# Optimization experiments

Hardware: AMD Instinct MI355X
Metric: run time of the kernel (lower is better)

## Reference

```python
import jax, jax.numpy as jnp
import numpy as np

# Constants from the torch module
S_DECAY = 0.95    # sentence_decay
P_DECAY = 0.99    # paragraph_decay
D_DECAY = 0.999   # document_decay
ALPHA = 0.1       # delta_update alpha for sentence/paragraph
DOC_ALPHA = 0.05  # delta_update alpha for document
BETA = 1.0
PARA_GROUP = 5    # sentences per paragraph
EPS = 1e-12       # F.normalize eps


def _normalize(x):
    # matches torch.nn.functional.normalize(x, dim=-1)
    return x / jnp.maximum(jnp.linalg.norm(x, axis=-1, keepdims=True), EPS)


def _delta_step(M, kn, v, alpha, beta):
    # M: [H, dk, dv]; kn: [dk] (already L2-normalized); v: [dv]
    # M_new = M @ (I - alpha * kn kn^T) + beta * kn v^T   (erase matrix is symmetric,
    # so the einsum 'hkv,hkj->hjv' form equals this rank-1 update -- no dk x dk matrix needed)
    kTM = jnp.einsum('k,hkv->hv', kn, M)                       # [H, dv]
    return M - alpha * kn[None, :, None] * kTM[:, None, :] \
             + beta * (kn[:, None] * v[None, :])[None, :, :]


def _scan_updates(M0, K, V, decay, alpha, beta):
    # Streaming delta-rule: per step, decay then erase/write.
    def step(M, kv):
        k, v = kv
        M = M * decay
        M = _delta_step(M, _normalize(k), v, alpha, beta)
        return M, None
    M, _ = jax.lax.scan(step, M0, (K, V))
    return M


def setup_inputs() -> dict:
    key = jax.random.key(0)
    ks = jax.random.split(key, 7)
    T, d_emb, d_k, d_v, H = 1000, 768, 256, 256, 8
    emb = jax.random.normal(ks[0], (T, d_emb), dtype=jnp.float32)
    q = jax.random.normal(ks[1], (d_k,), dtype=jnp.float32)
    W_k = jax.random.normal(ks[2], (d_emb, d_k), dtype=jnp.float32) * 0.02
    b_k = jax.random.normal(ks[3], (d_k,), dtype=jnp.float32) * 0.02
    W_v = jax.random.normal(ks[4], (d_emb, d_v), dtype=jnp.float32) * 0.02
    b_v = jax.random.normal(ks[5], (d_v,), dtype=jnp.float32) * 0.02
    M_sent0 = jnp.zeros((H, d_k, d_v), dtype=jnp.float32)
    M_para0 = jnp.zeros((H, d_k, d_v), dtype=jnp.float32)
    M_doc0 = jnp.zeros((H, d_k, d_v), dtype=jnp.float32)
    return {"emb": emb, "q": q, "W_k": W_k, "b_k": b_k, "W_v": W_v, "b_v": b_v,
            "M_sent0": M_sent0, "M_para0": M_para0, "M_doc0": M_doc0}


def reference(emb, q, W_k, b_k, W_v, b_v, M_sent0, M_para0, M_doc0):
    T, d_emb = emb.shape
    # Level 1: sentence memory -- one delta update per sentence embedding
    K = emb @ W_k + b_k            # [T, dk]
    V = emb @ W_v + b_v            # [T, dv]
    M_sent = _scan_updates(M_sent0, K, V, S_DECAY, ALPHA, BETA)
    # Level 2: paragraph memory -- mean of each group of 5 sentence embeddings
    para_emb = emb.reshape(T // PARA_GROUP, PARA_GROUP, d_emb).mean(axis=1)
    PK = para_emb @ W_k + b_k
    PV = para_emb @ W_v + b_v
    M_para = _scan_updates(M_para0, PK, PV, P_DECAY, ALPHA, BETA)
    # Level 3: document memory -- single update from paragraph-memory statistics
    doc_k = M_para.mean(axis=0).mean(axis=-1)   # [dk]
    doc_v = M_para.mean(axis=0).mean(axis=0)    # [dv]
    M_doc = M_doc0 * D_DECAY
    M_doc = _delta_step(M_doc, _normalize(doc_k), doc_v, DOC_ALPHA, BETA)
    # recall(q, level='all')
    qn = _normalize(q)
    def recall(M):
        return jnp.einsum('hkv,k->hv', M, qn).mean(axis=0)   # [dv]
    return 0.2 * recall(M_sent) + 0.3 * recall(M_para) + 0.5 * recall(M_doc)
```

## Files before the change

kernel.cpp:

```cpp
#include <hip/hip_runtime.h>
#include <hip/hip_bf16.h>

#define ALPHA   0.1f
#define S_DECAY 0.95f
#define P_DECAY 0.99f
#define D_EMB   768
#define DK      256

template<int ctrl, int row_mask>
__device__ __forceinline__ float dpp_add(float x) {
    int y = __builtin_amdgcn_update_dpp(0, __float_as_int(x), ctrl, row_mask, 0xF, true);
    return x + __int_as_float(y);
}

template<int N>
__device__ __forceinline__ void wave_allred_arr(float (&x)[N]) {
#pragma unroll
    for (int n = 0; n < N; ++n) x[n] = dpp_add<0xB1,  0xF>(x[n]);
#pragma unroll
    for (int n = 0; n < N; ++n) x[n] = dpp_add<0x4E,  0xF>(x[n]);
#pragma unroll
    for (int n = 0; n < N; ++n) x[n] = dpp_add<0x141, 0xF>(x[n]);
#pragma unroll
    for (int n = 0; n < N; ++n) x[n] = dpp_add<0x140, 0xF>(x[n]);
#pragma unroll
    for (int n = 0; n < N; ++n) x[n] = dpp_add<0x142, 0xA>(x[n]);
#pragma unroll
    for (int n = 0; n < N; ++n) x[n] = dpp_add<0x143, 0xC>(x[n]);
#pragma unroll
    for (int n = 0; n < N; ++n)
        x[n] = __int_as_float(__builtin_amdgcn_readlane(__float_as_int(x[n]), 63));
}

__device__ __forceinline__ float dot4v(const float4& a, const float4& b) {
    float t0 = a.x * b.x; t0 = fmaf(a.y, b.y, t0);
    float t1 = a.z * b.z; t1 = fmaf(a.w, b.w, t1);
    return t0 + t1;
}

__device__ __forceinline__ float rl(float x, int lane) {
    return __int_as_float(__builtin_amdgcn_readlane(__float_as_int(x), lane));
}

__global__ __launch_bounds__(256) void prep_kernel(
    const float* __restrict__ emb,
    const float* __restrict__ Wk, const float* __restrict__ bk,
    const float* __restrict__ Wv, const float* __restrict__ bv,
    float* __restrict__ K, float* __restrict__ V, float* __restrict__ USrev,
    float* __restrict__ out, int T)
{
    const int tid = threadIdx.x;
    const int bid = blockIdx.x;
    const int NBLK = (T / 4) * 2;
    if (bid >= NBLK) {
        const int PADS = ((T + 63) / 64) * 64;
        for (int i = tid; i < (PADS - T) * DK; i += 256) USrev[(size_t)T * DK + i] = 0.f;
        out[tid] = 0.f;
        return;
    }
    const int mat = bid & 1;
    const int r0  = (bid >> 1) * 4;

    __shared__ float se[4][D_EMB];
    __shared__ float s_red[4][4];

    const float4* emb4 = reinterpret_cast<const float4*>(emb);
#pragma unroll
    for (int r = 0; r < 4; ++r) {
        if (tid < D_EMB / 4)
            reinterpret_cast<float4*>(se[r])[tid] = emb4[(size_t)(r0 + r) * (D_EMB / 4) + tid];
    }
    __syncthreads();

    const float* Wp = mat ? Wv : Wk;
    const float* bp = mat ? bv : bk;
    const int j = tid;

    float a0 = 0.f, a1 = 0.f, a2 = 0.f, a3 = 0.f;
    float c0 = Wp[j],        c1 = Wp[j + DK],     c2 = Wp[j + 2*DK], c3 = Wp[j + 3*DK];
    float p0 = Wp[j + 4*DK], p1 = Wp[j + 5*DK],   p2 = Wp[j + 6*DK], p3 = Wp[j + 7*DK];

    for (int d = 0; d < D_EMB; d += 4) {
        int dn = d + 8; if (dn >= D_EMB) dn = 0;
        const float* wn = Wp + (size_t)dn * DK + j;
        float n0 = wn[0], n1 = wn[DK], n2 = wn[2*DK], n3 = wn[3*DK];

        float4 e0 = *reinterpret_cast<const float4*>(&se[0][d]);
        float4 e1 = *reinterpret_cast<const float4*>(&se[1][d]);
        float4 e2 = *reinterpret_cast<const float4*>(&se[2][d]);
        float4 e3 = *reinterpret_cast<const float4*>(&se[3][d]);

        a0 = fmaf(e0.x, c0, a0); a0 = fmaf(e0.y, c1, a0);
        a0 = fmaf(e0.z, c2, a0); a0 = fmaf(e0.w, c3, a0);
        a1 = fmaf(e1.x, c0, a1); a1 = fmaf(e1.y, c1, a1);
        a1 = fmaf(e1.z, c2, a1); a1 = fmaf(e1.w, c3, a1);
        a2 = fmaf(e2.x, c0, a2); a2 = fmaf(e2.y, c1, a2);
        a2 = fmaf(e2.z, c2, a2); a2 = fmaf(e2.w, c3, a2);
        a3 = fmaf(e3.x, c0, a3); a3 = fmaf(e3.y, c1, a3);
        a3 = fmaf(e3.z, c2, a3); a3 = fmaf(e3.w, c3, a3);

        c0 = p0; c1 = p1; c2 = p2; c3 = p3;
        p0 = n0; p1 = n1; p2 = n2; p3 = n3;
    }

    float bj = bp[j];
    float o0 = a0 + bj, o1 = a1 + bj, o2 = a2 + bj, o3 = a3 + bj;
    float* dst = mat ? V : K;
    dst[(size_t)(r0 + 0) * DK + j] = o0;
    dst[(size_t)(r0 + 1) * DK + j] = o1;
    dst[(size_t)(r0 + 2) * DK + j] = o2;
    dst[(size_t)(r0 + 3) * DK + j] = o3;

    if (mat == 0) {
        const int wave = tid >> 6, l = tid & 63;
        float red[4] = { o0*o0, o1*o1, o2*o2, o3*o3 };
        wave_allred_arr(red);
        if (l == 0) {
            s_red[wave][0] = red[0]; s_red[wave][1] = red[1];
            s_red[wave][2] = red[2]; s_red[wave][3] = red[3];
        }
        __syncthreads();
        float t0 = s_red[0][0] + s_red[1][0] + s_red[2][0] + s_red[3][0];
        float t1 = s_red[0][1] + s_red[1][1] + s_red[2][1] + s_red[3][1];
        float t2 = s_red[0][2] + s_red[1][2] + s_red[2][2] + s_red[3][2];
        float t3 = s_red[0][3] + s_red[1][3] + s_red[2][3] + s_red[3][3];
        USrev[(size_t)(T - 1 - (r0 + 0)) * DK + j] = o0 * (1.0f / fmaxf(sqrtf(t0), 1e-12f));
        USrev[(size_t)(T - 1 - (r0 + 1)) * DK + j] = o1 * (1.0f / fmaxf(sqrtf(t1), 1e-12f));
        USrev[(size_t)(T - 1 - (r0 + 2)) * DK + j] = o2 * (1.0f / fmaxf(sqrtf(t2), 1e-12f));
        USrev[(size_t)(T - 1 - (r0 + 3)) * DK + j] = o3 * (1.0f / fmaxf(sqrtf(t3), 1e-12f));
    }
}

__global__ __launch_bounds__(256) void ufill_kernel(
    const float* __restrict__ K, const float* __restrict__ V,
    float* __restrict__ UPrev, float* __restrict__ UPfwd,
    float* __restrict__ PV, float* __restrict__ SVv, float* __restrict__ F1,
    int P, int NCP)
{
    __shared__ float s_pd[64];
    __shared__ float4 s_f1w[4][64];
    const int tid = threadIdx.x, wv = tid >> 6, l = tid & 63;
    const int bid = blockIdx.x;
    const int type = (bid < NCP) ? 1 : 2;
    const int m = (type == 1) ? bid : bid - NCP;

    if (tid < 64) s_pd[tid] = powf(P_DECAY, (float)tid);
    __syncthreads();

    const float4* K4 = reinterpret_cast<const float4*>(K);

    if (type == 1) {
        for (int ii = 0; ii < 16; ++ii) {
            int i = wv * 16 + ii;
            int p = P - 1 - (64 * m + i);
            float4 u = make_float4(0.f, 0.f, 0.f, 0.f);
            if (p >= 0) {
                float4 pk = make_float4(0.f, 0.f, 0.f, 0.f);
#pragma unroll
                for (int s = 0; s < 5; ++s) {
                    float4 k4 = K4[(size_t)(5 * p + s) * 64 + l];
                    pk.x += k4.x; pk.y += k4.y; pk.z += k4.z; pk.w += k4.w;
                }
                pk.x *= 0.2f; pk.y *= 0.2f; pk.z *= 0.2f; pk.w *= 0.2f;
                float red[1] = { dot4v(pk, pk) };
                wave_allred_arr(red);
                float inv = 1.0f / fmaxf(sqrtf(red[0]), 1e-12f);
                u = make_float4(pk.x * inv, pk.y * inv, pk.z * inv, pk.w * inv);
            }
            reinterpret_cast<float4*>(UPrev)[(size_t)(64 * m + i) * 64 + l] = u;
        }
    } else {
        const float4* V4 = reinterpret_cast<const float4*>(V);
        float4 f1p = make_float4(0.f, 0.f, 0.f, 0.f);
        for (int ii = 0; ii < 16; ++ii) {
            int i = wv * 16 + ii;
            int p = 64 * m + i;
            float4 u = make_float4(0.f, 0.f, 0.f, 0.f);
            float sv = 0.f;
            if (p < P) {
                float4 pk = make_float4(0.f, 0.f, 0.f, 0.f);
                float4 pv = make_float4(0.f, 0.f, 0.f, 0.f);
#pragma unroll
                for (int s = 0; s < 5; ++s) {
                    float4 k4 = K4[(size_t)(5 * p + s) * 64 + l];
                    float4 v4 = V4[(size_t)(5 * p + s) * 64 + l];
                    pk.x += k4.x; pk.y += k4.y; pk.z += k4.z; pk.w += k4.w;
                    pv.x += v4.x; pv.y += v4.y; pv.z += v4.z; pv.w += v4.w;
                }
                pk.x *= 0.2f; pk.y *= 0.2f; pk.z *= 0.2f; pk.w *= 0.2f;
                pv.x *= 0.2f; pv.y *= 0.2f; pv.z *= 0.2f; pv.w *= 0.2f;
                reinterpret_cast<float4*>(PV)[(size_t)p * 64 + l] = pv;
                float red[2] = { dot4v(pk, pk), pv.x + pv.y + pv.z + pv.w };
                wave_allred_arr(red);
                float inv = 1.0f / fmaxf(sqrtf(red[0]), 1e-12f);
                u = make_float4(pk.x * inv, pk.y * inv, pk.z * inv, pk.w * inv);
                sv = red[1];
            }
            reinterpret_cast<float4*>(UPfwd)[(size_t)(64 * m + i) * 64 + l] = u;
            if (l == 0) SVv[64 * m + i] = sv;
            float f = s_pd[63 - i] * sv;
            f1p.x = fmaf(f, u.x, f1p.x); f1p.y = fmaf(f, u.y, f1p.y);
            f1p.z = fmaf(f, u.z, f1p.z); f1p.w = fmaf(f, u.w, f1p.w);
        }
        s_f1w[wv][l] = f1p;
        __syncthreads();
        if (wv == 0) {
            float4 a = s_f1w[0][l], b = s_f1w[1][l], c = s_f1w[2][l], d = s_f1w[3][l];
            float4 tot = make_float4(a.x+b.x+c.x+d.x, a.y+b.y+c.y+d.y,
                                     a.z+b.z+c.z+d.z, a.w+b.w+c.w+d.w);
            reinterpret_cast<float4*>(F1)[(size_t)m * 64 + l] = tot;
        }
    }
}

#define GS_STRIDE 260
__global__ __launch_bounds__(256) void gram_kernel(
    const float* __restrict__ USrev, const float* __restrict__ UPrev,
    const float* __restrict__ UPfwd, float* __restrict__ Agram,
    int NCS, int NCP)
{
    __shared__ float sAr[16 * GS_STRIDE];
    __shared__ float s_pd[64];
    const int tid = threadIdx.x;
    const int chunk = blockIdx.x >> 2;
    const int slab  = blockIdx.x & 3;
    int type, m;
    if (chunk < NCS)            { type = 0; m = chunk; }
    else if (chunk < NCS + NCP) { type = 1; m = chunk - NCS; }
    else                        { type = 2; m = chunk - NCS - NCP; }
    const float* Ug = (type == 0) ? USrev + (size_t)m * 64 * DK
                    : (type == 1) ? UPrev + (size_t)m * 64 * DK
                                  : UPfwd + (size_t)m * 64 * DK;
    const float4* Ug4 = reinterpret_cast<const float4*>(Ug);

    for (int idx = tid; idx < 16 * 64; idx += 256) {
        int r = idx >> 6, c4 = idx & 63;
        float4 t = Ug4[(size_t)(slab * 16 + r) * 64 + c4];
        *reinterpret_cast<float4*>(&sAr[r * GS_STRIDE + 4 * c4]) = t;
    }
    if (tid < 64) s_pd[tid] = powf(P_DECAY, (float)tid);
    __syncthreads();

    const int ti = tid & 15;
    const int tj = tid >> 4;
    const int gi = slab * 16 + ti;
    const int j0 = tj * 4;

    const float4* B0 = Ug4 + (size_t)(j0 + 0) * 64;
    const float4* B1 = Ug4 + (size_t)(j0 + 1) * 64;
    const float4* B2 = Ug4 + (size_t)(j0 + 2) * 64;
    const float4* B3 = Ug4 + (size_t)(j0 + 3) * 64;

    float g0 = 0.f, g1 = 0.f, g2 = 0.f, g3 = 0.f;
    for (int k4 = 0; k4 < 64; ++k4) {
        float4 a  = *reinterpret_cast<const float4*>(&sAr[ti * GS_STRIDE + 4 * k4]);
        float4 b0 = B0[k4], b1 = B1[k4], b2 = B2[k4], b3 = B3[k4];
        g0 += dot4v(a, b0); g1 += dot4v(a, b1);
        g2 += dot4v(a, b2); g3 += dot4v(a, b3);
    }

    float4 outv;
    outv.x = (j0 + 0 < gi) ? (ALPHA * g0 * ((type == 2) ? s_pd[gi - (j0 + 0)] : 1.f)) : 0.f;
    outv.y = (j0 + 1 < gi) ? (ALPHA * g1 * ((type == 2) ? s_pd[gi - (j0 + 1)] : 1.f)) : 0.f;
    outv.z = (j0 + 2 < gi) ? (ALPHA * g2 * ((type == 2) ? s_pd[gi - (j0 + 2)] : 1.f)) : 0.f;
    outv.w = (j0 + 3 < gi) ? (ALPHA * g3 * ((type == 2) ? s_pd[gi - (j0 + 3)] : 1.f)) : 0.f;
    reinterpret_cast<float4*>(Agram + (size_t)chunk * 4096)[gi * 16 + tj] = outv;
}

__global__ __launch_bounds__(256) void inv_kernel(
    float* __restrict__ AinvT, const float* __restrict__ SVv,
    float* __restrict__ biasF, int NCS, int NCP)
{
    __shared__ float sA[64 * 65];
    __shared__ float sX[64 * 65];
    __shared__ float s_sv[64];
    const int tid = threadIdx.x, wv = tid >> 6, l = tid & 63;
    const int bid = blockIdx.x;
    int type, m;
    if (bid < NCS)            { type = 0; m = bid; }
    else if (bid < NCS + NCP) { type = 1; m = bid - NCS; }
    else                      { type = 2; m = bid - NCS - NCP; }

    float* Ag = AinvT + (size_t)bid * 4096;
    for (int idx = tid; idx < 4096; idx += 256)
        sA[(idx >> 6) * 65 + (idx & 63)] = Ag[idx];
    if (type == 2 && tid < 64) s_sv[tid] = SVv[m * 64 + tid];
    __syncthreads();

    if (type == 2 && wv == 0) {
        float dotb = 0.f;
#pragma unroll
        for (int jj = 0; jj < 64; ++jj)
            dotb = fmaf(sA[l * 65 + jj], s_sv[jj], dotb);
        biasF[m * 64 + l] = dotb * (1.0f / ALPHA);
    }

    {
        const int base = wv * 16;
        float x[16];
#pragma unroll
        for (int r = 0; r < 16; ++r) x[r] = (base + r == l) ? 1.f : 0.f;
        for (int s = 0; s < 4; ++s) {
            if (wv == s) {
#pragma unroll
                for (int i = 1; i < 16; ++i)
#pragma unroll
                    for (int jj = 0; jj < 16; ++jj)
                        if (jj < i)
                            x[i] = fmaf(-sA[(base + i) * 65 + (base + jj)], x[jj], x[i]);
#pragma unroll
                for (int r = 0; r < 16; ++r) sX[(base + r) * 65 + l] = x[r];
            }
            __syncthreads();
            if (wv > s) {
#pragma unroll
                for (int i = 0; i < 16; ++i) {
                    float xi = sX[(s * 16 + i) * 65 + l];
#pragma unroll
                    for (int r = 0; r < 16; ++r)
                        x[r] = fmaf(-sA[(base + r) * 65 + (s * 16 + i)], xi, x[r]);
                }
            }
        }
    }
    __syncthreads();

    for (int idx = tid; idx < 4096; idx += 256) {
        int jcol = idx >> 6, irow = idx & 63;
        Ag[idx] = sX[irow * 65 + jcol];
    }
}

__global__ __launch_bounds__(512) void solve_kernel(
    const float* __restrict__ USrev, const float* __restrict__ UPrev,
    const float* __restrict__ UPfwd, const float* __restrict__ AinvT,
    const float* __restrict__ F1, const float* __restrict__ biasF,
    const float* __restrict__ q,
    float* __restrict__ BS, float* __restrict__ BPB1, float* __restrict__ BPB2,
    float* __restrict__ gscal, int NCS, int NCP)
{
    __shared__ float s_cp[8][64], s_cp2[8][64];
    __shared__ float4 s_part[8][64], s_part2[8][64];
    __shared__ float s_powd[65];
    const int tid = threadIdx.x, wave = tid >> 6, l = tid & 63;
    const int wb = wave * 8;
    if (tid <= 64) s_powd[tid] = powf(P_DECAY, (float)tid);

    float4 q4 = reinterpret_cast<const float4*>(q)[l];
    float qs[1] = { dot4v(q4, q4) };
    wave_allred_arr(qs);
    float qinv = 1.0f / fmaxf(sqrtf(qs[0]), 1e-12f);
    float4 qn = make_float4(q4.x * qinv, q4.y * qinv, q4.z * qinv, q4.w * qinv);
    __syncthreads();

    if (blockIdx.x == 0) {
        float4 w1 = qn;
        const float4* U4 = reinterpret_cast<const float4*>(USrev);
        float4 curU[8]; float curX[8];
#pragma unroll
        for (int r = 0; r < 8; ++r) {
            curU[r] = U4[(size_t)(wb + r) * 64 + l];
            curX[r] = AinvT[(size_t)(wb + r) * 64 + l];
        }
        for (int m = 0; m < NCS; ++m) {
            float4 nxtU[8]; float nxtX[8];
            if (m + 1 < NCS) {
#pragma unroll
                for (int r = 0; r < 8; ++r) {
                    nxtU[r] = U4[(size_t)(m + 1) * 4096 + (size_t)(wb + r) * 64 + l];
                    nxtX[r] = AinvT[(size_t)(m + 1) * 4096 + (size_t)(wb + r) * 64 + l];
                }
            }
            float d[8];
#pragma unroll
            for (int r = 0; r < 8; ++r) d[r] = dot4v(curU[r], w1);
            wave_allred_arr(d);
            if (l == 0) {
#pragma unroll
                for (int r = 0; r < 8; ++r) BS[m * 64 + wb + r] = d[r];
            }
            float cp = 0.f;
#pragma unroll
            for (int r = 0; r < 8; ++r) cp = fmaf(curX[r], d[r], cp);
            s_cp[wave][l] = cp;
            __syncthreads();
            float cl = 0.f;
#pragma unroll
            for (int w = 0; w < 8; ++w) cl += s_cp[w][l];
            float4 part = make_float4(0.f, 0.f, 0.f, 0.f);
#pragma unroll
            for (int r = 0; r < 8; ++r) {
                float ci = rl(cl, wb + r);
                part.x = fmaf(ci, curU[r].x, part.x); part.y = fmaf(ci, curU[r].y, part.y);
                part.z = fmaf(ci, curU[r].z, part.z); part.w = fmaf(ci, curU[r].w, part.w);
            }
            s_part[wave][l] = part;
            __syncthreads();
            float4 s = make_float4(0.f, 0.f, 0.f, 0.f);
#pragma unroll
            for (int w = 0; w < 8; ++w) {
                float4 p = s_part[w][l];
                s.x += p.x; s.y += p.y; s.z += p.z; s.w += p.w;
            }
            w1.x = fmaf(-ALPHA, s.x, w1.x); w1.y = fmaf(-ALPHA, s.y, w1.y);
            w1.z = fmaf(-ALPHA, s.z, w1.z); w1.w = fmaf(-ALPHA, s.w, w1.w);
            if (m + 1 < NCS) {
#pragma unroll
                for (int r = 0; r < 8; ++r) { curU[r] = nxtU[r]; curX[r] = nxtX[r]; }
            }
        }
    } else {
        {
            float4 w1 = qn;
            float4 w2 = make_float4(1.f, 1.f, 1.f, 1.f);
            const float4* U4 = reinterpret_cast<const float4*>(UPrev);
            float4 curU[8]; float curX[8];
#pragma unroll
            for (int r = 0; r < 8; ++r) {
                curU[r] = U4[(size_t)(wb + r) * 64 + l];
                curX[r] = AinvT[(size_t)NCS * 4096 + (size_t)(wb + r) * 64 + l];
            }
            for (int m = 0; m < NCP; ++m) {
                float4 nxtU[8]; float nxtX[8];
                if (m + 1 < NCP) {
#pragma unroll
                    for (int r = 0; r < 8; ++r) {
                        nxtU[r] = U4[(size_t)(m + 1) * 4096 + (size_t)(wb + r) * 64 + l];
                        nxtX[r] = AinvT[(size_t)(NCS + m + 1) * 4096 + (size_t)(wb + r) * 64 + l];
                    }
                }
                float d[16];
#pragma unroll
                for (int r = 0; r < 8; ++r) {
                    d[r]     = dot4v(curU[r], w1);
                    d[8 + r] = dot4v(curU[r], w2);
                }
                wave_allred_arr(d);
                if (l == 0) {
#pragma unroll
                    for (int r = 0; r < 8; ++r) {
                        BPB1[m * 64 + wb + r] = d[r];
                        BPB2[m * 64 + wb + r] = d[8 + r];
                    }
                }
                float cp1 = 0.f, cp2 = 0.f;
#pragma unroll
                for (int r = 0; r < 8; ++r) {
                    cp1 = fmaf(curX[r], d[r], cp1);
                    cp2 = fmaf(curX[r], d[8 + r], cp2);
                }
                s_cp[wave][l] = cp1; s_cp2[wave][l] = cp2;
                __syncthreads();
                float cl1 = 0.f, cl2 = 0.f;
#pragma unroll
                for (int w = 0; w < 8; ++w) { cl1 += s_cp[w][l]; cl2 += s_cp2[w][l]; }
                float4 p1 = make_float4(0.f,0.f,0.f,0.f), p2 = make_float4(0.f,0.f,0.f,0.f);
#pragma unroll
                for (int r = 0; r < 8; ++r) {
                    float c1 = rl(cl1, wb + r), c2 = rl(cl2, wb + r);
                    p1.x = fmaf(c1, curU[r].x, p1.x); p1.y = fmaf(c1, curU[r].y, p1.y);
                    p1.z = fmaf(c1, curU[r].z, p1.z); p1.w = fmaf(c1, curU[r].w, p1.w);
                    p2.x = fmaf(c2, curU[r].x, p2.x); p2.y = fmaf(c2, curU[r].y, p2.y);
                    p2.z = fmaf(c2, curU[r].z, p2.z); p2.w = fmaf(c2, curU[r].w, p2.w);
                }
                s_part[wave][l] = p1; s_part2[wave][l] = p2;
                __syncthreads();
                float4 s1 = make_float4(0.f,0.f,0.f,0.f), s2 = make_float4(0.f,0.f,0.f,0.f);
#pragma unroll
                for (int w = 0; w < 8; ++w) {
                    float4 a = s_part[w][l];  float4 b = s_part2[w][l];
                    s1.x += a.x; s1.y += a.y; s1.z += a.z; s1.w += a.w;
                    s2.x += b.x; s2.y += b.y; s2.z += b.z; s2.w += b.w;
                }
                w1.x = fmaf(-ALPHA, s1.x, w1.x); w1.y = fmaf(-ALPHA, s1.y, w1.y);
                w1.z = fmaf(-ALPHA, s1.z, w1.z); w1.w = fmaf(-ALPHA, s1.w, w1.w);
                w2.x = fmaf(-ALPHA, s2.x, w2.x); w2.y = fmaf(-ALPHA, s2.y, w2.y);
                w2.z = fmaf(-ALPHA, s2.z, w2.z); w2.w = fmaf(-ALPHA, s2.w, w2.w);
                if (m + 1 < NCP) {
#pragma unroll
                    for (int r = 0; r < 8; ++r) { curU[r] = nxtU[r]; curX[r] = nxtX[r]; }
                }
            }
        }
        __syncthreads();
        float4 y = make_float4(0.f, 0.f, 0.f, 0.f);
        {
            const float4* U4 = reinterpret_cast<const float4*>(UPfwd);
            float4 curU[8]; float curX[8];
#pragma unroll
            for (int r = 0; r < 8; ++r) {
                curU[r] = U4[(size_t)(wb + r) * 64 + l];
                curX[r] = AinvT[(size_t)(NCS + NCP) * 4096 + (size_t)(wb + r) * 64 + l];
            }
            for (int m = 0; m < NCP; ++m) {
                float4 nxtU[8]; float nxtX[8];
                if (m + 1 < NCP) {
#pragma unroll
                    for (int r = 0; r < 8; ++r) {
                        nxtU[r] = U4[(size_t)(m + 1) * 4096 + (size_t)(wb + r) * 64 + l];
                        nxtX[r] = AinvT[(size_t)(NCS + NCP + m + 1) * 4096 + (size_t)(wb + r) * 64 + l];
                    }
                }
                float biasr[8];
#pragma unroll
                for (int r = 0; r < 8; ++r) biasr[r] = biasF[m * 64 + wb + r];
                float4 f1 = reinterpret_cast<const float4*>(F1)[(size_t)m * 64 + l];
                float d[8];
#pragma unroll
                for (int r = 0; r < 8; ++r) d[r] = dot4v(curU[r], y);
                wave_allred_arr(d);
#pragma unroll
                for (int r = 0; r < 8; ++r)
                    d[r] = fmaf(s_powd[wb + r + 1], d[r], biasr[r]);
                float cp = 0.f;
#pragma unroll
                for (int r = 0; r < 8; ++r) cp = fmaf(curX[r], d[r], cp);
                s_cp[wave][l] = cp;
                __syncthreads();
                float cl = 0.f;
#pragma unroll
                for (int w = 0; w < 8; ++w) cl += s_cp[w][l];
                float4 part = make_float4(0.f, 0.f, 0.f, 0.f);
#pragma unroll
                for (int r = 0; r < 8; ++r) {
                    float ci = s_powd[63 - (wb + r)] * rl(cl, wb + r);
                    part.x = fmaf(ci, curU[r].x, part.x); part.y = fmaf(ci, curU[r].y, part.y);
                    part.z = fmaf(ci, curU[r].z, part.z); part.w = fmaf(ci, curU[r].w, part.w);
                }
                s_part[wave][l] = part;
                __syncthreads();
                float4 s = make_float4(0.f, 0.f, 0.f, 0.f);
#pragma unroll
                for (int w = 0; w < 8; ++w) {
                    float4 p = s_part[w][l];
                    s.x += p.x; s.y += p.y; s.z += p.z; s.w += p.w;
                }
                float d64 = s_powd[64];
                y.x = fmaf(d64, y.x, fmaf(-ALPHA, s.x, f1.x));
                y.y = fmaf(d64, y.y, fmaf(-ALPHA, s.y, f1.y));
                y.z = fmaf(d64, y.z, fmaf(-ALPHA, s.z, f1.z));
                y.w = fmaf(d64, y.w, fmaf(-ALPHA, s.w, f1.w));
                if (m + 1 < NCP) {
#pragma unroll
                    for (int r = 0; r < 8; ++r) { curU[r] = nxtU[r]; curX[r] = nxtX[r]; }
                }
            }
        }
        float fin[2] = { dot4v(y, y), dot4v(qn, y) };
        wave_allred_arr(fin);
        if (tid == 0) gscal[0] = fin[1] / fmaxf(sqrtf(fin[0]), 2.56e-10f);
    }
}

__global__ __launch_bounds__(256) void accum_kernel(
    const float* __restrict__ V, const float* __restrict__ PV,
    const float* __restrict__ AinvT,
    const float* __restrict__ BS, const float* __restrict__ BPB1,
    const float* __restrict__ BPB2, const float* __restrict__ gscal,
    float* __restrict__ out, int T, int P, int NCS, int NCP)
{
    __shared__ float s_b[64], s_cp[4][64], wc[64];
    const int b = blockIdx.x, t = threadIdx.x;
    const float* src; const float* B; int i0, realN, chunk, ci; float decay;
    if (b < NCS)            { src = V;  B = BS;   ci = b;             realN = T; decay = S_DECAY; chunk = b; }
    else if (b < NCS + NCP) { src = PV; B = BPB1; ci = b - NCS;       realN = P; decay = P_DECAY; chunk = b; }
    else                    { src = PV; B = BPB2; ci = b - NCS - NCP; realN = P; decay = P_DECAY; chunk = b - NCP; }
    i0 = ci * 64;
    if (t < 64) s_b[t] = B[ci * 64 + t];
    __syncthreads();
    {
        const int part = t >> 6, k = t & 63;
        const float* Xc = AinvT + (size_t)chunk * 4096;
        float cp = 0.f;
#pragma unroll
        for (int jj = 0; jj < 16; ++jj) {
            int j = part * 16 + jj;
            cp = fmaf(Xc[j * 64 + k], s_b[j], cp);
        }
        s_cp[part][k] = cp;
    }
    __syncthreads();
    if (t < 64) {
        float c = s_cp[0][t] + s_cp[1][t] + s_cp[2][t] + s_cp[3][t];
        wc[t] = powf(decay, (float)(i0 + t)) * c;
    }
    __syncthreads();
    const int k = t;
    float acc = 0.f;
    for (int ii = 0; ii < 64; ++ii) {
        int i = i0 + ii;
        if (i < realN)
            acc = fmaf(wc[ii], src[(size_t)(realN - 1 - i) * DK + k], acc);
    }
    float wlev;
    if (b < NCS)            wlev = 0.2f;
    else if (b < NCS + NCP) wlev = 0.3f;
    else                    wlev = (0.5f / 256.0f) * gscal[0];
    atomicAdd(&out[k], wlev * acc);
}

extern "C" void kernel_launch(void* const* d_in, const int* in_sizes, int n_in,
                              void* d_out, int out_size, void* d_ws, size_t ws_size,
                              hipStream_t stream) {
    const float* emb = (const float*)d_in[0];
    const float* q   = (const float*)d_in[1];
    const float* Wk  = (const float*)d_in[2];
    const float* bk  = (const float*)d_in[3];
    const float* Wv  = (const float*)d_in[4];
    const float* bv  = (const float*)d_in[5];

    const int T = in_sizes[0] / D_EMB;
    const int P = T / 5;
    const int NCS  = (T + 63) / 64;
    const int NCP  = (P + 63) / 64;
    const int PADS = NCS * 64;
    const int PADP = NCP * 64;
    const int NCH  = NCS + 2 * NCP;

    float* ws    = (float*)d_ws;
    float* K     = ws;
    float* V     = K     + (size_t)T * DK;
    float* PV    = V     + (size_t)T * DK;
    float* USrev = PV    + (size_t)PADP * DK;
    float* UPrev = USrev + (size_t)PADS * DK;
    float* UPfwd = UPrev + (size_t)PADP * DK;
    float* SVv   = UPfwd + (size_t)PADP * DK;
    float* AinvT = SVv   + PADP;
    float* F1    = AinvT + (size_t)NCH * 4096;
    float* biasF = F1    + (size_t)NCP * 256;
    float* BS    = biasF + PADP;
    float* BPB1  = BS    + PADS;
    float* BPB2  = BPB1  + PADP;
    float* gscal = BPB2  + PADP;

    prep_kernel<<<(T / 4) * 2 + 1, 256, 0, stream>>>(emb, Wk, bk, Wv, bv,
                                                     K, V, USrev, (float*)d_out, T);
    ufill_kernel<<<2 * NCP, 256, 0, stream>>>(K, V, UPrev, UPfwd, PV, SVv, F1, P, NCP);
    gram_kernel<<<NCH * 4, 256, 0, stream>>>(USrev, UPrev, UPfwd, AinvT, NCS, NCP);
    inv_kernel<<<NCH, 256, 0, stream>>>(AinvT, SVv, biasF, NCS, NCP);
    solve_kernel<<<2, 512, 0, stream>>>(USrev, UPrev, UPfwd, AinvT, F1, biasF, q,
                                        BS, BPB1, BPB2, gscal, NCS, NCP);
    accum_kernel<<<NCH, 256, 0, stream>>>(V, PV, AinvT, BS, BPB1, BPB2, gscal,
                                          (float*)d_out, T, P, NCS, NCP);
}
```

Baseline: 202.0 us.

## Fuse post-prep kernels into one cooperative kernel with grid syncs

Merges the ufill, gram, inverse, solve and accumulate stages into a single cooperative launch of 512-thread blocks, with grid-wide barriers between stages and one shared-memory buffer reused across them. The goal is to remove the launch and inter-kernel gap overhead of four separate small launches. If the cooperative launch fails, it falls back to the original separate kernels. The trade-offs are the cost of grid-wide syncs, many idle threads in phases that use 256 threads or only two blocks, and lower occupancy from the larger shared allocation.

```diff
diff --git a/kernel.cpp b/kernel.cpp
--- a/kernel.cpp
+++ b/kernel.cpp
@@ -1,5 +1,8 @@
 #include <hip/hip_runtime.h>
 #include <hip/hip_bf16.h>
+#include <hip/hip_cooperative_groups.h>
+
+namespace cg = cooperative_groups;
 
 #define ALPHA   0.1f
 #define S_DECAY 0.95f
@@ -131,16 +134,14 @@
     }
 }
 
-__global__ __launch_bounds__(256) void ufill_kernel(
-    const float* __restrict__ K, const float* __restrict__ V,
-    float* __restrict__ UPrev, float* __restrict__ UPfwd,
-    float* __restrict__ PV, float* __restrict__ SVv, float* __restrict__ F1,
-    int P, int NCP)
-{
-    __shared__ float s_pd[64];
-    __shared__ float4 s_f1w[4][64];
-    const int tid = threadIdx.x, wv = tid >> 6, l = tid & 63;
-    const int bid = blockIdx.x;
+
+__device__ __forceinline__ void ufill_body(int bid, int tid, char* smemc,
+    const float* K, const float* V, float* UPrev, float* UPfwd,
+    float* PV, float* SVv, float* F1, int P, int NCP)
+{
+    float*  s_pd  = (float*)smemc;
+    float4* s_f1w = (float4*)(smemc + 256);
+    const int wv = tid >> 6, l = tid & 63;
     const int type = (bid < NCP) ? 1 : 2;
     const int m = (type == 1) ? bid : bid - NCP;
 
@@ -150,62 +151,67 @@
     const float4* K4 = reinterpret_cast<const float4*>(K);
 
     if (type == 1) {
-        for (int ii = 0; ii < 16; ++ii) {
-            int i = wv * 16 + ii;
-            int p = P - 1 - (64 * m + i);
-            float4 u = make_float4(0.f, 0.f, 0.f, 0.f);
-            if (p >= 0) {
-                float4 pk = make_float4(0.f, 0.f, 0.f, 0.f);
-#pragma unroll
-                for (int s = 0; s < 5; ++s) {
-                    float4 k4 = K4[(size_t)(5 * p + s) * 64 + l];
-                    pk.x += k4.x; pk.y += k4.y; pk.z += k4.z; pk.w += k4.w;
-                }
-                pk.x *= 0.2f; pk.y *= 0.2f; pk.z *= 0.2f; pk.w *= 0.2f;
-                float red[1] = { dot4v(pk, pk) };
-                wave_allred_arr(red);
-                float inv = 1.0f / fmaxf(sqrtf(red[0]), 1e-12f);
-                u = make_float4(pk.x * inv, pk.y * inv, pk.z * inv, pk.w * inv);
-            }
-            reinterpret_cast<float4*>(UPrev)[(size_t)(64 * m + i) * 64 + l] = u;
+        if (tid < 256) {
+            for (int ii = 0; ii < 16; ++ii) {
+                int i = wv * 16 + ii;
+                int p = P - 1 - (64 * m + i);
+                float4 u = make_float4(0.f, 0.f, 0.f, 0.f);
+                if (p >= 0) {
+                    float4 pk = make_float4(0.f, 0.f, 0.f, 0.f);
+#pragma unroll
+                    for (int s = 0; s < 5; ++s) {
+                        float4 k4 = K4[(size_t)(5 * p + s) * 64 + l];
+                        pk.x += k4.x; pk.y += k4.y; pk.z += k4.z; pk.w += k4.w;
+                    }
+                    pk.x *= 0.2f; pk.y *= 0.2f; pk.z *= 0.2f; pk.w *= 0.2f;
+                    float red[1] = { dot4v(pk, pk) };
+                    wave_allred_arr(red);
+                    float inv = 1.0f / fmaxf(sqrtf(red[0]), 1e-12f);
+                    u = make_float4(pk.x * inv, pk.y * inv, pk.z * inv, pk.w * inv);
+                }
+                reinterpret_cast<float4*>(UPrev)[(size_t)(64 * m + i) * 64 + l] = u;
+            }
         }
     } else {
         const float4* V4 = reinterpret_cast<const float4*>(V);
-        float4 f1p = make_float4(0.f, 0.f, 0.f, 0.f);
-        for (int ii = 0; ii < 16; ++ii) {
-            int i = wv * 16 + ii;
-            int p = 64 * m + i;
-            float4 u = make_float4(0.f, 0.f, 0.f, 0.f);
-            float sv = 0.f;
-            if (p < P) {
-                float4 pk = make_float4(0.f, 0.f, 0.f, 0.f);
-                float4 pv = make_float4(0.f, 0.f, 0.f, 0.f);
-#pragma unroll
-                for (int s = 0; s < 5; ++s) {
-                    float4 k4 = K4[(size_t)(5 * p + s) * 64 + l];
-                    float4 v4 = V4[(size_t)(5 * p + s) * 64 + l];
-                    pk.x += k4.x; pk.y += k4.y; pk.z += k4.z; pk.w += k4.w;
-                    pv.x += v4.x; pv.y += v4.y; pv.z += v4.z; pv.w += v4.w;
-                }
-                pk.x *= 0.2f; pk.y *= 0.2f; pk.z *= 0.2f; pk.w *= 0.2f;
-                pv.x *= 0.2f; pv.y *= 0.2f; pv.z *= 0.2f; pv.w *= 0.2f;
-                reinterpret_cast<float4*>(PV)[(size_t)p * 64 + l] = pv;
-                float red[2] = { dot4v(pk, pk), pv.x + pv.y + pv.z + pv.w };
-                wave_allred_arr(red);
-                float inv = 1.0f / fmaxf(sqrtf(red[0]), 1e-12f);
-                u = make_float4(pk.x * inv, pk.y * inv, pk.z * inv, pk.w * inv);
-                sv = red[1];
-            }
-            reinterpret_cast<float4*>(UPfwd)[(size_t)(64 * m + i) * 64 + l] = u;
-            if (l == 0) SVv[64 * m + i] = sv;
-            float f = s_pd[63 - i] * sv;
-            f1p.x = fmaf(f, u.x, f1p.x); f1p.y = fmaf(f, u.y, f1p.y);
-            f1p.z = fmaf(f, u.z, f1p.z); f1p.w = fmaf(f, u.w, f1p.w);
-        }
-        s_f1w[wv][l] = f1p;
+        if (tid < 256) {
+            float4 f1p = make_float4(0.f, 0.f, 0.f, 0.f);
+            for (int ii = 0; ii < 16; ++ii) {
+                int i = wv * 16 + ii;
+                int p = 64 * m + i;
+                float4 u = make_float4(0.f, 0.f, 0.f, 0.f);
+                float sv = 0.f;
+                if (p < P) {
+                    float4 pk = make_float4(0.f, 0.f, 0.f, 0.f);
+                    float4 pv = make_float4(0.f, 0.f, 0.f, 0.f);
+#pragma unroll
+                    for (int s = 0; s < 5; ++s) {
+                        float4 k4 = K4[(size_t)(5 * p + s) * 64 + l];
+                        float4 v4 = V4[(size_t)(5 * p + s) * 64 + l];
+                        pk.x += k4.x; pk.y += k4.y; pk.z += k4.z; pk.w += k4.w;
+                        pv.x += v4.x; pv.y += v4.y; pv.z += v4.z; pv.w += v4.w;
+                    }
+                    pk.x *= 0.2f; pk.y *= 0.2f; pk.z *= 0.2f; pk.w *= 0.2f;
+                    pv.x *= 0.2f; pv.y *= 0.2f; pv.z *= 0.2f; pv.w *= 0.2f;
+                    reinterpret_cast<float4*>(PV)[(size_t)p * 64 + l] = pv;
+                    float red[2] = { dot4v(pk, pk), pv.x + pv.y + pv.z + pv.w };
+                    wave_allred_arr(red);
+                    float inv = 1.0f / fmaxf(sqrtf(red[0]), 1e-12f);
+                    u = make_float4(pk.x * inv, pk.y * inv, pk.z * inv, pk.w * inv);
+                    sv = red[1];
+                }
+                reinterpret_cast<float4*>(UPfwd)[(size_t)(64 * m + i) * 64 + l] = u;
+                if (l == 0) SVv[64 * m + i] = sv;
+                float f = s_pd[63 - i] * sv;
+                f1p.x = fmaf(f, u.x, f1p.x); f1p.y = fmaf(f, u.y, f1p.y);
+                f1p.z = fmaf(f, u.z, f1p.z); f1p.w = fmaf(f, u.w, f1p.w);
+            }
+            s_f1w[wv * 64 + l] = f1p;
+        }
         __syncthreads();
-        if (wv == 0) {
-            float4 a = s_f1w[0][l], b = s_f1w[1][l], c = s_f1w[2][l], d = s_f1w[3][l];
+        if (tid < 64) {
+            float4 a = s_f1w[0 * 64 + l], b = s_f1w[1 * 64 + l];
+            float4 c = s_f1w[2 * 64 + l], d = s_f1w[3 * 64 + l];
             float4 tot = make_float4(a.x+b.x+c.x+d.x, a.y+b.y+c.y+d.y,
                                      a.z+b.z+c.z+d.z, a.w+b.w+c.w+d.w);
             reinterpret_cast<float4*>(F1)[(size_t)m * 64 + l] = tot;
@@ -214,16 +220,14 @@
 }
 
 #define GS_STRIDE 260
-__global__ __launch_bounds__(256) void gram_kernel(
-    const float* __restrict__ USrev, const float* __restrict__ UPrev,
-    const float* __restrict__ UPfwd, float* __restrict__ Agram,
+__device__ __forceinline__ void gram_body(int gb, int tid, int nthr, char* smemc,
+    const float* USrev, const float* UPrev, const float* UPfwd, float* Agram,
     int NCS, int NCP)
 {
-    __shared__ float sAr[16 * GS_STRIDE];
-    __shared__ float s_pd[64];
-    const int tid = threadIdx.x;
-    const int chunk = blockIdx.x >> 2;
-    const int slab  = blockIdx.x & 3;
+    float* sAr  = (float*)smemc;
+    float* s_pd = sAr + 16 * GS_STRIDE;
+    const int chunk = gb >> 2;
+    const int slab  = gb & 3;
     int type, m;
     if (chunk < NCS)            { type = 0; m = chunk; }
     else if (chunk < NCS + NCP) { type = 1; m = chunk - NCS; }
@@ -233,7 +237,7 @@
                                   : UPfwd + (size_t)m * 64 * DK;
     const float4* Ug4 = reinterpret_cast<const float4*>(Ug);
 
-    for (int idx = tid; idx < 16 * 64; idx += 256) {
+    for (int idx = tid; idx < 16 * 64; idx += nthr) {
         int r = idx >> 6, c4 = idx & 63;
         float4 t = Ug4[(size_t)(slab * 16 + r) * 64 + c4];
         *reinterpret_cast<float4*>(&sAr[r * GS_STRIDE + 4 * c4]) = t;
@@ -241,48 +245,48 @@
     if (tid < 64) s_pd[tid] = powf(P_DECAY, (float)tid);
     __syncthreads();
 
-    const int ti = tid & 15;
-    const int tj = tid >> 4;
-    const int gi = slab * 16 + ti;
-    const int j0 = tj * 4;
-
-    const float4* B0 = Ug4 + (size_t)(j0 + 0) * 64;
-    const float4* B1 = Ug4 + (size_t)(j0 + 1) * 64;
-    const float4* B2 = Ug4 + (size_t)(j0 + 2) * 64;
-    const float4* B3 = Ug4 + (size_t)(j0 + 3) * 64;
-
-    float g0 = 0.f, g1 = 0.f, g2 = 0.f, g3 = 0.f;
-    for (int k4 = 0; k4 < 64; ++k4) {
-        float4 a  = *reinterpret_cast<const float4*>(&sAr[ti * GS_STRIDE + 4 * k4]);
-        float4 b0 = B0[k4], b1 = B1[k4], b2 = B2[k4], b3 = B3[k4];
-        g0 += dot4v(a, b0); g1 += dot4v(a, b1);
-        g2 += dot4v(a, b2); g3 += dot4v(a, b3);
-    }
-
-    float4 outv;
-    outv.x = (j0 + 0 < gi) ? (ALPHA * g0 * ((type == 2) ? s_pd[gi - (j0 + 0)] : 1.f)) : 0.f;
-    outv.y = (j0 + 1 < gi) ? (ALPHA * g1 * ((type == 2) ? s_pd[gi - (j0 + 1)] : 1.f)) : 0.f;
-    outv.z = (j0 + 2 < gi) ? (ALPHA * g2 * ((type == 2) ? s_pd[gi - (j0 + 2)] : 1.f)) : 0.f;
-    outv.w = (j0 + 3 < gi) ? (ALPHA * g3 * ((type == 2) ? s_pd[gi - (j0 + 3)] : 1.f)) : 0.f;
-    reinterpret_cast<float4*>(Agram + (size_t)chunk * 4096)[gi * 16 + tj] = outv;
-}
-
-__global__ __launch_bounds__(256) void inv_kernel(
-    float* __restrict__ AinvT, const float* __restrict__ SVv,
-    float* __restrict__ biasF, int NCS, int NCP)
-{
-    __shared__ float sA[64 * 65];
-    __shared__ float sX[64 * 65];
-    __shared__ float s_sv[64];
-    const int tid = threadIdx.x, wv = tid >> 6, l = tid & 63;
-    const int bid = blockIdx.x;
+    if (tid < 256) {
+        const int ti = tid & 15;
+        const int tj = tid >> 4;
+        const int gi = slab * 16 + ti;
+        const int j0 = tj * 4;
+
+        const float4* B0 = Ug4 + (size_t)(j0 + 0) * 64;
+        const float4* B1 = Ug4 + (size_t)(j0 + 1) * 64;
+        const float4* B2 = Ug4 + (size_t)(j0 + 2) * 64;
+        const float4* B3 = Ug4 + (size_t)(j0 + 3) * 64;
+
+        float g0 = 0.f, g1 = 0.f, g2 = 0.f, g3 = 0.f;
+        for (int k4 = 0; k4 < 64; ++k4) {
+            float4 a  = *reinterpret_cast<const float4*>(&sAr[ti * GS_STRIDE + 4 * k4]);
+            float4 b0 = B0[k4], b1 = B1[k4], b2 = B2[k4], b3 = B3[k4];
+            g0 += dot4v(a, b0); g1 += dot4v(a, b1);
+            g2 += dot4v(a, b2); g3 += dot4v(a, b3);
+        }
+
+        float4 outv;
+        outv.x = (j0 + 0 < gi) ? (ALPHA * g0 * ((type == 2) ? s_pd[gi - (j0 + 0)] : 1.f)) : 0.f;
+        outv.y = (j0 + 1 < gi) ? (ALPHA * g1 * ((type == 2) ? s_pd[gi - (j0 + 1)] : 1.f)) : 0.f;
+        outv.z = (j0 + 2 < gi) ? (ALPHA * g2 * ((type == 2) ? s_pd[gi - (j0 + 2)] : 1.f)) : 0.f;
+        outv.w = (j0 + 3 < gi) ? (ALPHA * g3 * ((type == 2) ? s_pd[gi - (j0 + 3)] : 1.f)) : 0.f;
+        reinterpret_cast<float4*>(Agram + (size_t)chunk * 4096)[gi * 16 + tj] = outv;
+    }
+}
+
+__device__ __forceinline__ void inv_body(int bid, int tid, int nthr, char* smemc,
+    float* AinvT, const float* SVv, float* biasF, int NCS, int NCP)
+{
+    float* sA   = (float*)smemc;
+    float* sX   = sA + 64 * 65;
+    float* s_sv = sX + 64 * 65;
+    const int wv = tid >> 6, l = tid & 63;
     int type, m;
     if (bid < NCS)            { type = 0; m = bid; }
     else if (bid < NCS + NCP) { type = 1; m = bid - NCS; }
     else                      { type = 2; m = bid - NCS - NCP; }
 
     float* Ag = AinvT + (size_t)bid * 4096;
-    for (int idx = tid; idx < 4096; idx += 256)
+    for (int idx = tid; idx < 4096; idx += nthr)
         sA[(idx >> 6) * 65 + (idx & 63)] = Ag[idx];
     if (type == 2 && tid < 64) s_sv[tid] = SVv[m * 64 + tid];
     __syncthreads();
@@ -296,10 +300,10 @@
     }
 
     {
-        const int base = wv * 16;
+        const int base = (wv & 3) * 16;
         float x[16];
 #pragma unroll
-        for (int r = 0; r < 16; ++r) x[r] = (base + r == l) ? 1.f : 0.f;
+        for (int r = 0; r < 16; ++r) x[r] = (base + r == l && wv < 4) ? 1.f : 0.f;
         for (int s = 0; s < 4; ++s) {
             if (wv == s) {
 #pragma unroll
@@ -312,7 +316,7 @@
                 for (int r = 0; r < 16; ++r) sX[(base + r) * 65 + l] = x[r];
             }
             __syncthreads();
-            if (wv > s) {
+            if (wv > s && wv < 4) {
 #pragma unroll
                 for (int i = 0; i < 16; ++i) {
                     float xi = sX[(s * 16 + i) * 65 + l];
@@ -325,24 +329,23 @@
     }
     __syncthreads();
 
-    for (int idx = tid; idx < 4096; idx += 256) {
+    for (int idx = tid; idx < 4096; idx += nthr) {
         int jcol = idx >> 6, irow = idx & 63;
         Ag[idx] = sX[irow * 65 + jcol];
     }
 }
 
-__global__ __launch_bounds__(512) void solve_kernel(
-    const float* __restrict__ USrev, const float* __restrict__ UPrev,
-    const float* __restrict__ UPfwd, const float* __restrict__ AinvT,
-    const float* __restrict__ F1, const float* __restrict__ biasF,
-    const float* __restrict__ q,
-    float* __restrict__ BS, float* __restrict__ BPB1, float* __restrict__ BPB2,
-    float* __restrict__ gscal, int NCS, int NCP)
-{
-    __shared__ float s_cp[8][64], s_cp2[8][64];
-    __shared__ float4 s_part[8][64], s_part2[8][64];
-    __shared__ float s_powd[65];
-    const int tid = threadIdx.x, wave = tid >> 6, l = tid & 63;
+__device__ __forceinline__ void solve_body(int bid, int tid, char* smemc,
+    const float* USrev, const float* UPrev, const float* UPfwd, const float* AinvT,
+    const float* F1, const float* biasF, const float* q,
+    float* BS, float* BPB1, float* BPB2, float* gscal, int NCS, int NCP)
+{
+    float*  s_cp    = (float*)smemc;
+    float*  s_cp2   = s_cp + 512;
+    float4* s_part  = (float4*)(smemc + 4096);
+    float4* s_part2 = s_part + 512;
+    float*  s_powd  = (float*)(smemc + 20480);
+    const int wave = tid >> 6, l = tid & 63;
     const int wb = wave * 8;
     if (tid <= 64) s_powd[tid] = powf(P_DECAY, (float)tid);
 
@@ -353,7 +356,7 @@
     float4 qn = make_float4(q4.x * qinv, q4.y * qinv, q4.z * qinv, q4.w * qinv);
     __syncthreads();
 
-    if (blockIdx.x == 0) {
+    if (bid == 0) {
         float4 w1 = qn;
         const float4* U4 = reinterpret_cast<const float4*>(USrev);
         float4 curU[8]; float curX[8];
@@ -382,11 +385,11 @@
             float cp = 0.f;
 #pragma unroll
             for (int r = 0; r < 8; ++r) cp = fmaf(curX[r], d[r], cp);
-            s_cp[wave][l] = cp;
+            s_cp[wave * 64 + l] = cp;
             __syncthreads();
             float cl = 0.f;
 #pragma unroll
-            for (int w = 0; w < 8; ++w) cl += s_cp[w][l];
+            for (int w = 0; w < 8; ++w) cl += s_cp[w * 64 + l];
             float4 part = make_float4(0.f, 0.f, 0.f, 0.f);
 #pragma unroll
             for (int r = 0; r < 8; ++r) {
@@ -394,12 +397,12 @@
                 part.x = fmaf(ci, curU[r].x, part.x); part.y = fmaf(ci, curU[r].y, part.y);
                 part.z = fmaf(ci, curU[r].z, part.z); part.w = fmaf(ci, curU[r].w, part.w);
             }
-            s_part[wave][l] = part;
+            s_part[wave * 64 + l] = part;
             __syncthreads();
             float4 s = make_float4(0.f, 0.f, 0.f, 0.f);
 #pragma unroll
             for (int w = 0; w < 8; ++w) {
-                float4 p = s_part[w][l];
+                float4 p = s_part[w * 64 + l];
                 s.x += p.x; s.y += p.y; s.z += p.z; s.w += p.w;
             }
             w1.x = fmaf(-ALPHA, s.x, w1.x); w1.y = fmaf(-ALPHA, s.y, w1.y);
@@ -409,7 +412,7 @@
                 for (int r = 0; r < 8; ++r) { curU[r] = nxtU[r]; curX[r] = nxtX[r]; }
             }
         }
-    } else {
+    } else if (bid == 1) {
         {
             float4 w1 = qn;
             float4 w2 = make_float4(1.f, 1.f, 1.f, 1.f);
@@ -449,11 +452,11 @@
                     cp1 = fmaf(curX[r], d[r], cp1);
                     cp2 = fmaf(curX[r], d[8 + r], cp2);
                 }
-                s_cp[wave][l] = cp1; s_cp2[wave][l] = cp2;
+                s_cp[wave * 64 + l] = cp1; s_cp2[wave * 64 + l] = cp2;
                 __syncthreads();
                 float cl1 = 0.f, cl2 = 0.f;
 #pragma unroll
-                for (int w = 0; w < 8; ++w) { cl1 += s_cp[w][l]; cl2 += s_cp2[w][l]; }
+                for (int w = 0; w < 8; ++w) { cl1 += s_cp[w * 64 + l]; cl2 += s_cp2[w * 64 + l]; }
                 float4 p1 = make_float4(0.f,0.f,0.f,0.f), p2 = make_float4(0.f,0.f,0.f,0.f);
 #pragma unroll
                 for (int r = 0; r < 8; ++r) {
@@ -463,12 +466,12 @@
                     p2.x = fmaf(c2, curU[r].x, p2.x); p2.y = fmaf(c2, curU[r].y, p2.y);
                     p2.z = fmaf(c2, curU[r].z, p2.z); p2.w = fmaf(c2, curU[r].w, p2.w);
                 }
-                s_part[wave][l] = p1; s_part2[wave][l] = p2;
+                s_part[wave * 64 + l] = p1; s_part2[wave * 64 + l] = p2;
                 __syncthreads();
                 float4 s1 = make_float4(0.f,0.f,0.f,0.f), s2 = make_float4(0.f,0.f,0.f,0.f);
 #pragma unroll
                 for (int w = 0; w < 8; ++w) {
-                    float4 a = s_part[w][l];  float4 b = s_part2[w][l];
+                    float4 a = s_part[w * 64 + l];  float4 b = s_part2[w * 64 + l];
                     s1.x += a.x; s1.y += a.y; s1.z += a.z; s1.w += a.w;
                     s2.x += b.x; s2.y += b.y; s2.z += b.z; s2.w += b.w;
                 }
@@ -515,11 +518,11 @@
                 float cp = 0.f;
 #pragma unroll
                 for (int r = 0; r < 8; ++r) cp = fmaf(curX[r], d[r], cp);
-                s_cp[wave][l] = cp;
+                s_cp[wave * 64 + l] = cp;
                 __syncthreads();
                 float cl = 0.f;
 #pragma unroll
-                for (int w = 0; w < 8; ++w) cl += s_cp[w][l];
+                for (int w = 0; w < 8; ++w) cl += s_cp[w * 64 + l];
                 float4 part = make_float4(0.f, 0.f, 0.f, 0.f);
 #pragma unroll
                 for (int r = 0; r < 8; ++r) {
@@ -527,12 +530,12 @@
                     part.x = fmaf(ci, curU[r].x, part.x); part.y = fmaf(ci, curU[r].y, part.y);
                     part.z = fmaf(ci, curU[r].z, part.z); part.w = fmaf(ci, curU[r].w, part.w);
                 }
-                s_part[wave][l] = part;
+                s_part[wave * 64 + l] = part;
                 __syncthreads();
                 float4 s = make_float4(0.f, 0.f, 0.f, 0.f);
 #pragma unroll
                 for (int w = 0; w < 8; ++w) {
-                    float4 p = s_part[w][l];
+                    float4 p = s_part[w * 64 + l];
                     s.x += p.x; s.y += p.y; s.z += p.z; s.w += p.w;
                 }
                 float d64 = s_powd[64];
@@ -552,15 +555,14 @@
     }
 }
 
-__global__ __launch_bounds__(256) void accum_kernel(
-    const float* __restrict__ V, const float* __restrict__ PV,
-    const float* __restrict__ AinvT,
-    const float* __restrict__ BS, const float* __restrict__ BPB1,
-    const float* __restrict__ BPB2, const float* __restrict__ gscal,
-    float* __restrict__ out, int T, int P, int NCS, int NCP)
-{
-    __shared__ float s_b[64], s_cp[4][64], wc[64];
-    const int b = blockIdx.x, t = threadIdx.x;
+__device__ __forceinline__ void accum_body(int b, int t, char* smemc,
+    const float* V, const float* PV, const float* AinvT,
+    const float* BS, const float* BPB1, const float* BPB2, const float* gscal,
+    float* out, int T, int P, int NCS, int NCP)
+{
+    float* s_b  = (float*)smemc;
+    float* s_cp = s_b + 64;
+    float* wc   = s_cp + 256;
     const float* src; const float* B; int i0, realN, chunk, ci; float decay;
     if (b < NCS)            { src = V;  B = BS;   ci = b;             realN = T; decay = S_DECAY; chunk = b; }
     else if (b < NCS + NCP) { src = PV; B = BPB1; ci = b - NCS;       realN = P; decay = P_DECAY; chunk = b; }
@@ -568,7 +570,7 @@
     i0 = ci * 64;
     if (t < 64) s_b[t] = B[ci * 64 + t];
     __syncthreads();
-    {
+    if (t < 256) {
         const int part = t >> 6, k = t & 63;
         const float* Xc = AinvT + (size_t)chunk * 4096;
         float cp = 0.f;
@@ -577,26 +579,105 @@
             int j = part * 16 + jj;
             cp = fmaf(Xc[j * 64 + k], s_b[j], cp);
         }
-        s_cp[part][k] = cp;
+        s_cp[part * 64 + k] = cp;
     }
     __syncthreads();
     if (t < 64) {
-        float c = s_cp[0][t] + s_cp[1][t] + s_cp[2][t] + s_cp[3][t];
+        float c = s_cp[0 * 64 + t] + s_cp[1 * 64 + t] + s_cp[2 * 64 + t] + s_cp[3 * 64 + t];
         wc[t] = powf(decay, (float)(i0 + t)) * c;
     }
     __syncthreads();
-    const int k = t;
-    float acc = 0.f;
-    for (int ii = 0; ii < 64; ++ii) {
-        int i = i0 + ii;
-        if (i < realN)
-            acc = fmaf(wc[ii], src[(size_t)(realN - 1 - i) * DK + k], acc);
-    }
-    float wlev;
-    if (b < NCS)            wlev = 0.2f;
-    else if (b < NCS + NCP) wlev = 0.3f;
-    else                    wlev = (0.5f / 256.0f) * gscal[0];
-    atomicAdd(&out[k], wlev * acc);
+    if (t < 256) {
+        const int k = t;
+        float acc = 0.f;
+        for (int ii = 0; ii < 64; ++ii) {
+            int i = i0 + ii;
+            if (i < realN)
+                acc = fmaf(wc[ii], src[(size_t)(realN - 1 - i) * DK + k], acc);
+        }
+        float wlev;
+        if (b < NCS)            wlev = 0.2f;
+        else if (b < NCS + NCP) wlev = 0.3f;
+        else                    wlev = (0.5f / 256.0f) * gscal[0];
+        atomicAdd(&out[k], wlev * acc);
+    }
+}
+
+__global__ __launch_bounds__(512) void coop_kernel(
+    const float* K, const float* V, const float* USrev,
+    float* UPrev, float* UPfwd, float* PV, float* SVv,
+    float* AinvT, float* F1, float* biasF,
+    const float* q, float* BS, float* BPB1, float* BPB2, float* gscal,
+    float* out, int T, int P, int NCS, int NCP)
+{
+    cg::grid_group grid = cg::this_grid();
+    __shared__ __align__(16) char smem[33536];
+    const int bid = blockIdx.x, tid = threadIdx.x;
+    const int NCH = NCS + 2 * NCP;
+
+    if (bid < 2 * NCP)
+        ufill_body(bid, tid, smem, K, V, UPrev, UPfwd, PV, SVv, F1, P, NCP);
+    grid.sync();
+
+    if (bid < NCH * 4)
+        gram_body(bid, tid, 512, smem, USrev, UPrev, UPfwd, AinvT, NCS, NCP);
+    grid.sync();
+
+    if (bid < NCH)
+        inv_body(bid, tid, 512, smem, AinvT, SVv, biasF, NCS, NCP);
+    grid.sync();
+
+    if (bid < 2)
+        solve_body(bid, tid, smem, USrev, UPrev, UPfwd, AinvT, F1, biasF, q,
+                   BS, BPB1, BPB2, gscal, NCS, NCP);
+    grid.sync();
+
+    if (bid < NCH)
+        accum_body(bid, tid, smem, V, PV, AinvT, BS, BPB1, BPB2, gscal,
+                   out, T, P, NCS, NCP);
+}
+
+__global__ __launch_bounds__(256) void ufill_kernel(
+    const float* K, const float* V, float* UPrev, float* UPfwd,
+    float* PV, float* SVv, float* F1, int P, int NCP)
+{
+    __shared__ __align__(16) char sm[4352];
+    ufill_body(blockIdx.x, threadIdx.x, sm, K, V, UPrev, UPfwd, PV, SVv, F1, P, NCP);
+}
+
+__global__ __launch_bounds__(256) void gram_kernel(
+    const float* USrev, const float* UPrev, const float* UPfwd, float* Agram,
+    int NCS, int NCP)
+{
+    __shared__ __align__(16) char sm[16896];
+    gram_body(blockIdx.x, threadIdx.x, 256, sm, USrev, UPrev, UPfwd, Agram, NCS, NCP);
+}
+
+__global__ __launch_bounds__(256) void inv_kernel(
+    float* AinvT, const float* SVv, float* biasF, int NCS, int NCP)
+{
+    __shared__ __align__(16) char sm[33536];
+    inv_body(blockIdx.x, threadIdx.x, 256, sm, AinvT, SVv, biasF, NCS, NCP);
+}
+
+__global__ __launch_bounds__(512) void solve_kernel(
+    const float* USrev, const float* UPrev, const float* UPfwd, const float* AinvT,
+    const float* F1, const float* biasF, const float* q,
+    float* BS, float* BPB1, float* BPB2, float* gscal, int NCS, int NCP)
+{
+    __shared__ __align__(16) char sm[20752];
+    solve_body(blockIdx.x, threadIdx.x, sm, USrev, UPrev, UPfwd, AinvT, F1, biasF, q,
+               BS, BPB1, BPB2, gscal, NCS, NCP);
+}
+
+__global__ __launch_bounds__(256) void accum_kernel(
+    const float* V, const float* PV, const float* AinvT,
+    const float* BS, const float* BPB1, const float* BPB2, const float* gscal,
+    float* out, int T, int P, int NCS, int NCP)
+{
+    __shared__ __align__(16) char sm[1536];
+    accum_body(blockIdx.x, threadIdx.x, sm, V, PV, AinvT, BS, BPB1, BPB2, gscal,
+               out, T, P, NCS, NCP);
 }
 
 extern "C" void kernel_launch(void* const* d_in, const int* in_sizes, int n_in,
@@ -632,14 +713,27 @@
     float* BPB1  = BS    + PADS;
     float* BPB2  = BPB1  + PADP;
     float* gscal = BPB2  + PADP;
+    float* outp  = (float*)d_out;
 
     prep_kernel<<<(T / 4) * 2 + 1, 256, 0, stream>>>(emb, Wk, bk, Wv, bv,
-                                                     K, V, USrev, (float*)d_out, T);
-    ufill_kernel<<<2 * NCP, 256, 0, stream>>>(K, V, UPrev, UPfwd, PV, SVv, F1, P, NCP);
-    gram_kernel<<<NCH * 4, 256, 0, stream>>>(USrev, UPrev, UPfwd, AinvT, NCS, NCP);
-    inv_kernel<<<NCH, 256, 0, stream>>>(AinvT, SVv, biasF, NCS, NCP);
-    solve_kernel<<<2, 512, 0, stream>>>(USrev, UPrev, UPfwd, AinvT, F1, biasF, q,
-                                        BS, BPB1, BPB2, gscal, NCS, NCP);
-    accum_kernel<<<NCH, 256, 0, stream>>>(V, PV, AinvT, BS, BPB1, BPB2, gscal,
-                                          (float*)d_out, T, P, NCS, NCP);
-}
+                                                     K, V, USrev, outp, T);
+
+    void* cargs[] = {
+        (void*)&K, (void*)&V, (void*)&USrev, (void*)&UPrev, (void*)&UPfwd,
+        (void*)&PV, (void*)&SVv, (void*)&AinvT, (void*)&F1, (void*)&biasF,
+        (void*)&q, (void*)&BS, (void*)&BPB1, (void*)&BPB2, (void*)&gscal,
+        (void*)&outp, (void*)&T, (void*)&P, (void*)&NCS, (void*)&NCP
+    };
+    hipError_t cerr = hipLaunchCooperativeKernel((const void*)coop_kernel,
+                                                 dim3(NCH * 4), dim3(512),
+                                                 cargs, 0, stream);
+    if (cerr != hipSuccess) {
+        ufill_kernel<<<2 * NCP, 256, 0, stream>>>(K, V, UPrev, UPfwd, PV, SVv, F1, P, NCP);
+        gram_kernel<<<NCH * 4, 256, 0, stream>>>(USrev, UPrev, UPfwd, AinvT, NCS, NCP);
+        inv_kernel<<<NCH, 256, 0, stream>>>(AinvT, SVv, biasF, NCS, NCP);
+        solve_kernel<<<2, 512, 0, stream>>>(USrev, UPrev, UPfwd, AinvT, F1, biasF, q,
+                                            BS, BPB1, BPB2, gscal, NCS, NCP);
+        accum_kernel<<<NCH, 256, 0, stream>>>(V, PV, AinvT, BS, BPB1, BPB2, gscal,
+                                              outp, T, P, NCS, NCP);
+    }
+}
```

New measurement: 237.9 us. +17.8%, slower.
